# Optimization experiments

Hardware: AMD Instinct MI355X
Metric: run time of the kernel (lower is better)

The kernel has to match this reference:

```python
import jax, jax.numpy as jnp
import numpy as np

N_NODES = 50000
N_EDGES = 600000


def gcn_conv(x, src, dst, W, b, num_nodes):
    # x: [N, Cin] -> [N, Cout]; symmetric-normalized GCN with self-loops
    h = x @ W  # [N, Cout]
    loop = jnp.arange(num_nodes, dtype=src.dtype)
    s = jnp.concatenate([src, loop])
    d = jnp.concatenate([dst, loop])
    ones = jnp.ones(s.shape[0], dtype=h.dtype)
    deg = jax.ops.segment_sum(ones, d, num_segments=num_nodes)  # in-degree incl self-loop
    dinv = jnp.where(deg > 0, jax.lax.rsqrt(deg), 0.0)
    norm = dinv[s] * dinv[d]  # [E+N]
    msg = h[s] * norm[:, None]  # gather + scale
    out = jax.ops.segment_sum(msg, d, num_segments=num_nodes)  # scatter-add
    return out + b


def setup_inputs() -> dict:
    key = jax.random.key(0)
    k1, k2, k3, k4 = jax.random.split(key, 4)
    x = jax.random.normal(k1, (N_NODES, 128), dtype=jnp.float32)
    edge_index = jax.random.randint(k2, (2, N_EDGES), 0, N_NODES, dtype=jnp.int64)
    W1 = jax.random.normal(k3, (128, 128), dtype=jnp.float32) * (1.0 / np.sqrt(128))
    b1 = jnp.zeros((128,), dtype=jnp.float32)
    W2 = jax.random.normal(k4, (128, 64), dtype=jnp.float32) * (1.0 / np.sqrt(128))
    b2 = jnp.zeros((64,), dtype=jnp.float32)
    return {"x": x, "edge_index": edge_index, "W1": W1, "b1": b1, "W2": W2, "b2": b2}


def reference(x, edge_index, W1, b1, W2, b2):
    src, dst = edge_index[0], edge_index[1]
    h = gcn_conv(x, src, dst, W1, b1, N_NODES)
    h = jax.nn.relu(h)
    out = gcn_conv(h, src, dst, W2, b2, N_NODES)
    return out
```

## Files before the change

kernel.cpp:

```cpp
#include <hip/hip_runtime.h>
#include <cstddef>
#include <cstdint>

#define N_NODES 50000
#define N_EDGES 600000
#define M_TILES 3125
#define GEMM_BLKS 782
#define NBUCK 196
#define BUCK_CAP 4096
#define K1_BLKS 147
#define K1_EDGES 4096

typedef short bf16x8 __attribute__((ext_vector_type(8)));
typedef float f32x4 __attribute__((ext_vector_type(4)));


__device__ __forceinline__ unsigned short f32_to_bf16(float x) {
  unsigned u = __float_as_uint(x);
  u += 0x7FFFu + ((u >> 16) & 1u);
  return (unsigned short)(u >> 16);
}
__device__ __forceinline__ float bf16_to_f32(unsigned short h) {
  return __uint_as_float((unsigned)h << 16);
}
__device__ __forceinline__ float bf16_lo(unsigned g) {
  return __uint_as_float(g << 16);
}
__device__ __forceinline__ float bf16_hi(unsigned g) {
  return __uint_as_float(g & 0xFFFF0000u);
}

__device__ __forceinline__ void split8(const float* __restrict__ p, bf16x8& hi,
                                       bf16x8& lo) {
  const float4 v0 = *(const float4*)p;
  const float4 v1 = *(const float4*)(p + 4);
  float v[8] = {v0.x, v0.y, v0.z, v0.w, v1.x, v1.y, v1.z, v1.w};
#pragma unroll
  for (int i = 0; i < 8; i++) {
    const unsigned short h = f32_to_bf16(v[i]);
    hi[i] = (short)h;
    lo[i] = (short)f32_to_bf16(v[i] - bf16_to_f32(h));
  }
}

__global__ __launch_bounds__(256) void k_prep(
    const float* __restrict__ W1, const float* __restrict__ W2,
    unsigned short* __restrict__ w1h, unsigned short* __restrict__ w1l,
    unsigned short* __restrict__ w2h, unsigned short* __restrict__ w2l,
    int* __restrict__ cursor) {
  const int b = blockIdx.x;
  const int tid = threadIdx.x;
  if (b < 96) {
    const int i = b * 256 + tid;
    const float* W;
    unsigned short *wh, *wl;
    int o, cout;
    if (i < 16384) {
      W = W1; wh = w1h; wl = w1l; o = i; cout = 128;
    } else {
      W = W2; wh = w2h; wl = w2l; o = i - 16384; cout = 64;
    }
    const int j = o & 7;
    const int lane = (o >> 3) & 63;
    const int t = o >> 9;
    const int ks = t & 3;
    const int ct = t >> 2;
    const int k = ks * 32 + (lane >> 4) * 8 + j;
    const int n = ct * 16 + (lane & 15);
    const float v = W[k * cout + n];
    const unsigned short h = f32_to_bf16(v);
    wh[o] = h;
    wl[o] = f32_to_bf16(v - bf16_to_f32(h));
  } else {
    if (tid < NBUCK) cursor[tid] = tid * BUCK_CAP;
  }
}

template <int COUT>
__device__ __forceinline__ void gemm_body(const int wtile, const int lane,
                                          const float* __restrict__ X,
                                          const unsigned short* __restrict__ Wph,
                                          const unsigned short* __restrict__ Wpl,
                                          unsigned short* __restrict__ Hs) {
  constexpr int CT = COUT / 16;
  const int m = lane & 15;
  const int q = lane >> 4;

  f32x4 acc[CT];
#pragma unroll
  for (int ct = 0; ct < CT; ct++) acc[ct] = {0.f, 0.f, 0.f, 0.f};

  const float* xp = X + (size_t)(wtile * 16 + m) * 128 + q * 8;

#pragma unroll
  for (int ks = 0; ks < 4; ks++) {
    bf16x8 ah, al;
    split8(xp + ks * 32, ah, al);
#pragma unroll
    for (int ct = 0; ct < CT; ct++) {
      const size_t bo = ((size_t)(ct * 4 + ks) * 64 + lane) * 8;
      const bf16x8 bh = *(const bf16x8*)(Wph + bo);
      const bf16x8 bl = *(const bf16x8*)(Wpl + bo);
      acc[ct] = __builtin_amdgcn_mfma_f32_16x16x32_bf16(ah, bh, acc[ct], 0, 0, 0);
      acc[ct] = __builtin_amdgcn_mfma_f32_16x16x32_bf16(al, bh, acc[ct], 0, 0, 0);
      acc[ct] = __builtin_amdgcn_mfma_f32_16x16x32_bf16(ah, bl, acc[ct], 0, 0, 0);
    }
  }
#pragma unroll
  for (int ct = 0; ct < CT; ct++) {
#pragma unroll
    for (int r = 0; r < 4; r++) {
      const int orow = wtile * 16 + q * 4 + r;
      Hs[(size_t)orow * COUT + ct * 16 + m] = f32_to_bf16(acc[ct][r]);
    }
  }
}

__global__ __launch_bounds__(256) void k_route_gemm128(
    const float* __restrict__ X, const unsigned short* __restrict__ Wph,
    const unsigned short* __restrict__ Wpl, unsigned short* __restrict__ Hs,
    const int* __restrict__ src, const int* __restrict__ dst,
    int* __restrict__ cursor, unsigned* __restrict__ routed) {
  __shared__ int hist[NBUCK];
  __shared__ int lcur[NBUCK];
  const int tid = threadIdx.x;
  if (blockIdx.x < K1_BLKS) {
    for (int t = tid; t < NBUCK; t += 256) hist[t] = 0;
    __syncthreads();
    unsigned packed[16];
    bool cvalid[4];
    const int base = blockIdx.x * K1_EDGES;
#pragma unroll
    for (int c = 0; c < 4; c++) {
      const int i4 = base + c * 1024 + tid * 4;
      cvalid[c] = (i4 < N_EDGES);
      if (cvalid[c]) {
        const int4 d4 = *(const int4*)(dst + i4);
        const int4 s4 = *(const int4*)(src + i4);
        packed[c * 4 + 0] = ((unsigned)d4.x << 16) | (unsigned)s4.x;
        packed[c * 4 + 1] = ((unsigned)d4.y << 16) | (unsigned)s4.y;
        packed[c * 4 + 2] = ((unsigned)d4.z << 16) | (unsigned)s4.z;
        packed[c * 4 + 3] = ((unsigned)d4.w << 16) | (unsigned)s4.w;
#pragma unroll
        for (int j = 0; j < 4; j++)
          atomicAdd(&hist[packed[c * 4 + j] >> 24], 1);
      }
    }
    __syncthreads();
    for (int t = tid; t < NBUCK; t += 256)
      lcur[t] = atomicAdd(&cursor[t], hist[t]);
    __syncthreads();
#pragma unroll
    for (int c = 0; c < 4; c++) {
      if (cvalid[c]) {
#pragma unroll
        for (int j = 0; j < 4; j++) {
          const unsigned pk = packed[c * 4 + j];
          const int slot = atomicAdd(&lcur[pk >> 24], 1);
          routed[slot] = pk;
        }
      }
    }
  } else {
    const int wtile = (blockIdx.x - K1_BLKS) * 4 + (tid >> 6);
    if (wtile < M_TILES) gemm_body<128>(wtile, tid & 63, X, Wph, Wpl, Hs);
  }
}

__global__ __launch_bounds__(1024) void k_bsort(
    const unsigned* __restrict__ routed, const int* __restrict__ cursor,
    int* __restrict__ counts, int* __restrict__ start,
    int* __restrict__ sorted_src) {
  __shared__ unsigned ebuf[BUCK_CAP];
  __shared__ int h2[256];
  __shared__ int c2[256];
  const int b = blockIdx.x;
  const int tid = threadIdx.x;
  const int n = cursor[b] - b * BUCK_CAP;
  for (int i = tid; i < n; i += 1024) ebuf[i] = routed[b * BUCK_CAP + i];
  if (tid < 256) h2[tid] = 0;
  __syncthreads();
  for (int i = tid; i < n; i += 1024)
    atomicAdd(&h2[(ebuf[i] >> 16) & 255], 1);
  __syncthreads();
  int own = 0;
  if (tid < 256) own = h2[tid];
  for (int s = 1; s < 256; s <<= 1) {
    int t = 0;
    if (tid < 256 && tid >= s) t = h2[tid - s];
    __syncthreads();
    if (tid < 256) h2[tid] += t;
    __syncthreads();
  }
  if (tid < 256) {
    const int pfx = h2[tid] - own;
    c2[tid] = pfx;
    const int d = b * 256 + tid;
    if (d < N_NODES) {
      counts[d] = own;
      start[d] = b * BUCK_CAP + pfx;
    }
  }
  __syncthreads();
  for (int i = tid; i < n; i += 1024) {
    const unsigned pk = ebuf[i];
    const int r = atomicAdd(&c2[(pk >> 16) & 255], 1);
    sorted_src[b * BUCK_CAP + r] = (int)(pk & 0xFFFFu);
  }
}

__global__ __launch_bounds__(256) void k_agg128_gemm64(
    const unsigned* __restrict__ Hb, const int* __restrict__ counts,
    const int* __restrict__ start, const int* __restrict__ sorted_src,
    const float* __restrict__ bias, const unsigned short* __restrict__ Wph,
    const unsigned short* __restrict__ Wpl, unsigned short* __restrict__ Hs) {
  __shared__ float a1s[16][132];
  const int lane = threadIdx.x & 63;
  const int wave = threadIdx.x >> 6;
  const float2 bb = ((const float2*)bias)[lane];

  int deg[4], e0v[4];
  float dvv[4];
  unsigned gselfv[4];
  int siv[4];
  float wiv[4];
#pragma unroll
  for (int i = 0; i < 4; i++) {
    const int v = blockIdx.x * 16 + wave * 4 + i;
    deg[i] = counts[v];
    e0v[i] = start[v];
  }
#pragma unroll
  for (int i = 0; i < 4; i++) {
    const int v = blockIdx.x * 16 + wave * 4 + i;
    dvv[i] = rsqrtf((float)deg[i] + 1.0f);
    gselfv[i] = Hb[(size_t)v * 64 + lane];
    siv[i] = (lane < deg[i]) ? sorted_src[e0v[i] + lane] : 0;
  }
#pragma unroll
  for (int i = 0; i < 4; i++) {
    wiv[i] = (lane < deg[i]) ? rsqrtf((float)counts[siv[i]] + 1.0f) * dvv[i]
                             : 0.f;
  }

#pragma unroll
  for (int i = 0; i < 4; i++) {
    const int r = wave * 4 + i;
    const float dv = dvv[i];
    float ax = bf16_lo(gselfv[i]) * (dv * dv);
    float ay = bf16_hi(gselfv[i]) * (dv * dv);
    const int dg = min(deg[i], 64);

    int j = 0;
    for (; j + 8 <= dg; j += 8) {
      int s[8];
      float w[8];
      unsigned g[8];
#pragma unroll
      for (int t = 0; t < 8; t++) {
        s[t] = __shfl(siv[i], j + t);
        w[t] = __shfl(wiv[i], j + t);
      }
#pragma unroll
      for (int t = 0; t < 8; t++) g[t] = Hb[(size_t)s[t] * 64 + lane];
#pragma unroll
      for (int t = 0; t < 8; t++) {
        ax += bf16_lo(g[t]) * w[t];
        ay += bf16_hi(g[t]) * w[t];
      }
    }
    for (; j + 4 <= dg; j += 4) {
      int s[4];
      float w[4];
      unsigned g[4];
#pragma unroll
      for (int t = 0; t < 4; t++) {
        s[t] = __shfl(siv[i], j + t);
        w[t] = __shfl(wiv[i], j + t);
      }
#pragma unroll
      for (int t = 0; t < 4; t++) g[t] = Hb[(size_t)s[t] * 64 + lane];
#pragma unroll
      for (int t = 0; t < 4; t++) {
        ax += bf16_lo(g[t]) * w[t];
        ay += bf16_hi(g[t]) * w[t];
      }
    }
    for (; j < dg; j++) {
      const int s = __shfl(siv[i], j);
      const float w = __shfl(wiv[i], j);
      const unsigned g = Hb[(size_t)s * 64 + lane];
      ax += bf16_lo(g) * w;
      ay += bf16_hi(g) * w;
    }
    a1s[r][lane * 2] = fmaxf(ax + bb.x, 0.f);
    a1s[r][lane * 2 + 1] = fmaxf(ay + bb.y, 0.f);
  }
  __syncthreads();

  const int ct = wave;
  const int m = lane & 15;
  const int q = lane >> 4;
  f32x4 acc = {0.f, 0.f, 0.f, 0.f};
#pragma unroll
  for (int ks = 0; ks < 4; ks++) {
    bf16x8 ah, al;
    split8(&a1s[m][ks * 32 + q * 8], ah, al);
    const size_t bo = ((size_t)(ct * 4 + ks) * 64 + lane) * 8;
    const bf16x8 bh = *(const bf16x8*)(Wph + bo);
    const bf16x8 bl = *(const bf16x8*)(Wpl + bo);
    acc = __builtin_amdgcn_mfma_f32_16x16x32_bf16(ah, bh, acc, 0, 0, 0);
    acc = __builtin_amdgcn_mfma_f32_16x16x32_bf16(al, bh, acc, 0, 0, 0);
    acc = __builtin_amdgcn_mfma_f32_16x16x32_bf16(ah, bl, acc, 0, 0, 0);
  }
#pragma unroll
  for (int r = 0; r < 4; r++) {
    const int orow = blockIdx.x * 16 + q * 4 + r;
    Hs[(size_t)orow * 64 + ct * 16 + m] = f32_to_bf16(acc[r]);
  }
}

__global__ __launch_bounds__(256) void k_agg64(
    const unsigned* __restrict__ Hb, const int* __restrict__ counts,
    const int* __restrict__ start, const int* __restrict__ sorted_src,
    const float* __restrict__ bias, float* __restrict__ out) {
  const int hl = threadIdx.x & 31;
  const int hw = threadIdx.x >> 5;
  const int v0 = blockIdx.x * 16 + hw * 2;
  const float2 bb = ((const float2*)bias)[hl];

  int deg[2], e0v[2];
  float dvv[2];
  unsigned gs[2];
  int siv[2];
  float wiv[2];
#pragma unroll
  for (int i = 0; i < 2; i++) {
    const int v = v0 + i;
    deg[i] = counts[v];
    e0v[i] = start[v];
  }
#pragma unroll
  for (int i = 0; i < 2; i++) {
    const int v = v0 + i;
    dvv[i] = rsqrtf((float)deg[i] + 1.0f);
    gs[i] = Hb[(size_t)v * 32 + hl];
    siv[i] = (hl < deg[i]) ? sorted_src[e0v[i] + hl] : 0;
  }
#pragma unroll
  for (int i = 0; i < 2; i++) {
    wiv[i] = (hl < deg[i]) ? rsqrtf((float)counts[siv[i]] + 1.0f) * dvv[i]
                           : 0.f;
  }

#pragma unroll
  for (int i = 0; i < 2; i++) {
    const int v = v0 + i;
    const float dv = dvv[i];
    float ax = bf16_lo(gs[i]) * (dv * dv);
    float ay = bf16_hi(gs[i]) * (dv * dv);
    const int dg0 = min(deg[i], 32);

    int j = 0;
    for (; j + 8 <= dg0; j += 8) {
      int s[8];
      float w[8];
      unsigned g[8];
#pragma unroll
      for (int t = 0; t < 8; t++) {
        s[t] = __shfl(siv[i], j + t, 32);
        w[t] = __shfl(wiv[i], j + t, 32);
      }
#pragma unroll
      for (int t = 0; t < 8; t++) g[t] = Hb[(size_t)s[t] * 32 + hl];
#pragma unroll
      for (int t = 0; t < 8; t++) {
        ax += bf16_lo(g[t]) * w[t];
        ay += bf16_hi(g[t]) * w[t];
      }
    }
    for (; j + 4 <= dg0; j += 4) {
      int s[4];
      float w[4];
      unsigned g[4];
#pragma unroll
      for (int t = 0; t < 4; t++) {
        s[t] = __shfl(siv[i], j + t, 32);
        w[t] = __shfl(wiv[i], j + t, 32);
      }
#pragma unroll
      for (int t = 0; t < 4; t++) g[t] = Hb[(size_t)s[t] * 32 + hl];
#pragma unroll
      for (int t = 0; t < 4; t++) {
        ax += bf16_lo(g[t]) * w[t];
        ay += bf16_hi(g[t]) * w[t];
      }
    }
    for (; j < dg0; j++) {
      const int s = __shfl(siv[i], j, 32);
      const float w = __shfl(wiv[i], j, 32);
      const unsigned g = Hb[(size_t)s * 32 + hl];
      ax += bf16_lo(g) * w;
      ay += bf16_hi(g) * w;
    }
    for (int base = 32; base < deg[i]; base += 32) {
      const int cnt2 = min(32, deg[i] - base);
      int sit = 0;
      float wit = 0.f;
      if (base + hl < deg[i]) {
        sit = sorted_src[e0v[i] + base + hl];
        wit = rsqrtf((float)counts[sit] + 1.0f) * dv;
      }
      for (int k = 0; k < cnt2; k++) {
        const int s = __shfl(sit, k, 32);
        const float w = __shfl(wit, k, 32);
        const unsigned g = Hb[(size_t)s * 32 + hl];
        ax += bf16_lo(g) * w;
        ay += bf16_hi(g) * w;
      }
    }
    float2 r;
    r.x = ax + bb.x;
    r.y = ay + bb.y;
    ((float2*)out)[(size_t)v * 32 + hl] = r;
  }
}


extern "C" void kernel_launch(void* const* d_in, const int* in_sizes, int n_in,
                              void* d_out, int out_size, void* d_ws, size_t ws_size,
                              hipStream_t stream) {
  const float* x = (const float*)d_in[0];
  const int* ei = (const int*)d_in[1];
  const float* W1 = (const float*)d_in[2];
  const float* b1 = (const float*)d_in[3];
  const float* W2 = (const float*)d_in[4];
  const float* b2 = (const float*)d_in[5];
  const int* src = ei;
  const int* dst = ei + N_EDGES;

  char* p = (char*)d_ws;
  auto alloc = [&](size_t bytes) {
    char* q = p;
    p += (bytes + 255) & ~(size_t)255;
    return q;
  };
  int* cursor = (int*)alloc((size_t)NBUCK * 4);
  unsigned* routed = (unsigned*)alloc((size_t)NBUCK * BUCK_CAP * 4);
  int* sorted_src = (int*)alloc((size_t)NBUCK * BUCK_CAP * 4);
  int* counts = (int*)alloc((size_t)N_NODES * 4);
  int* start = (int*)alloc((size_t)N_NODES * 4);
  unsigned short* w1h = (unsigned short*)alloc(16384 * 2);
  unsigned short* w1l = (unsigned short*)alloc(16384 * 2);
  unsigned short* w2h = (unsigned short*)alloc(8192 * 2);
  unsigned short* w2l = (unsigned short*)alloc(8192 * 2);
  unsigned short* h1b = (unsigned short*)alloc((size_t)N_NODES * 128 * 2);
  unsigned short* h2b = (unsigned short*)alloc((size_t)N_NODES * 64 * 2);

  hipLaunchKernelGGL(k_prep, dim3(97), dim3(256), 0, stream, W1, W2, w1h, w1l,
                     w2h, w2l, cursor);
  hipLaunchKernelGGL(k_route_gemm128, dim3(K1_BLKS + GEMM_BLKS), dim3(256), 0,
                     stream, x, w1h, w1l, h1b, src, dst, cursor, routed);
  hipLaunchKernelGGL(k_bsort, dim3(NBUCK), dim3(1024), 0, stream, routed,
                     cursor, counts, start, sorted_src);
  hipLaunchKernelGGL(k_agg128_gemm64, dim3(M_TILES), dim3(256), 0, stream,
                     (const unsigned*)h1b, counts, start, sorted_src, b1, w2h,
                     w2l, h2b);
  hipLaunchKernelGGL(k_agg64, dim3(M_TILES), dim3(256), 0, stream,
                     (const unsigned*)h2b, counts, start, sorted_src, b2,
                     (float*)d_out);
}
```

Baseline: 152.4 us.

## Regroup kernels: route with prep, bucket sort with layer-1 GEMM, widen aggregation lanes

```diff
diff --git a/kernel.cpp b/kernel.cpp
--- a/kernel.cpp
+++ b/kernel.cpp
@@ -8,8 +8,8 @@
 #define GEMM_BLKS 782
 #define NBUCK 196
 #define BUCK_CAP 4096
-#define K1_BLKS 147
-#define K1_EDGES 4096
+#define ROUTE_EDGES 2048
+#define ROUTE_BLKS 293
 
 typedef short bf16x8 __attribute__((ext_vector_type(8)));
 typedef float f32x4 __attribute__((ext_vector_type(4)));
@@ -43,15 +43,57 @@
   }
 }
 
-__global__ __launch_bounds__(256) void k_prep(
+template <int COUT>
+__device__ __forceinline__ void gemm_body(const int wtile, const int lane,
+                                          const float* __restrict__ X,
+                                          const unsigned short* __restrict__ Wph,
+                                          const unsigned short* __restrict__ Wpl,
+                                          unsigned short* __restrict__ Hs) {
+  constexpr int CT = COUT / 16;
+  const int m = lane & 15;
+  const int q = lane >> 4;
+
+  f32x4 acc[CT];
+#pragma unroll
+  for (int ct = 0; ct < CT; ct++) acc[ct] = {0.f, 0.f, 0.f, 0.f};
+
+  const float* xp = X + (size_t)(wtile * 16 + m) * 128 + q * 8;
+
+#pragma unroll
+  for (int ks = 0; ks < 4; ks++) {
+    bf16x8 ah, al;
+    split8(xp + ks * 32, ah, al);
+#pragma unroll
+    for (int ct = 0; ct < CT; ct++) {
+      const size_t bo = ((size_t)(ct * 4 + ks) * 64 + lane) * 8;
+      const bf16x8 bh = *(const bf16x8*)(Wph + bo);
+      const bf16x8 bl = *(const bf16x8*)(Wpl + bo);
+      acc[ct] = __builtin_amdgcn_mfma_f32_16x16x32_bf16(ah, bh, acc[ct], 0, 0, 0);
+      acc[ct] = __builtin_amdgcn_mfma_f32_16x16x32_bf16(al, bh, acc[ct], 0, 0, 0);
+      acc[ct] = __builtin_amdgcn_mfma_f32_16x16x32_bf16(ah, bl, acc[ct], 0, 0, 0);
+    }
+  }
+#pragma unroll
+  for (int ct = 0; ct < CT; ct++) {
+#pragma unroll
+    for (int r = 0; r < 4; r++) {
+      const int orow = wtile * 16 + q * 4 + r;
+      Hs[(size_t)orow * COUT + ct * 16 + m] = f32_to_bf16(acc[ct][r]);
+    }
+  }
+}
+
+__global__ __launch_bounds__(256) void k_prep_route(
     const float* __restrict__ W1, const float* __restrict__ W2,
     unsigned short* __restrict__ w1h, unsigned short* __restrict__ w1l,
     unsigned short* __restrict__ w2h, unsigned short* __restrict__ w2l,
-    int* __restrict__ cursor) {
-  const int b = blockIdx.x;
+    const int* __restrict__ src, const int* __restrict__ dst,
+    int* __restrict__ cursor, unsigned* __restrict__ routed) {
+  __shared__ int hist[NBUCK];
+  __shared__ int lcur[NBUCK];
   const int tid = threadIdx.x;
-  if (b < 96) {
-    const int i = b * 256 + tid;
+  if (blockIdx.x < 96) {
+    const int i = blockIdx.x * 256 + tid;
     const float* W;
     unsigned short *wh, *wl;
     int o, cout;
@@ -72,66 +114,14 @@
     wh[o] = h;
     wl[o] = f32_to_bf16(v - bf16_to_f32(h));
   } else {
-    if (tid < NBUCK) cursor[tid] = tid * BUCK_CAP;
-  }
-}
-
-template <int COUT>
-__device__ __forceinline__ void gemm_body(const int wtile, const int lane,
-                                          const float* __restrict__ X,
-                                          const unsigned short* __restrict__ Wph,
-                                          const unsigned short* __restrict__ Wpl,
-                                          unsigned short* __restrict__ Hs) {
-  constexpr int CT = COUT / 16;
-  const int m = lane & 15;
-  const int q = lane >> 4;
-
-  f32x4 acc[CT];
-#pragma unroll
-  for (int ct = 0; ct < CT; ct++) acc[ct] = {0.f, 0.f, 0.f, 0.f};
-
-  const float* xp = X + (size_t)(wtile * 16 + m) * 128 + q * 8;
-
-#pragma unroll
-  for (int ks = 0; ks < 4; ks++) {
-    bf16x8 ah, al;
-    split8(xp + ks * 32, ah, al);
-#pragma unroll
-    for (int ct = 0; ct < CT; ct++) {
-      const size_t bo = ((size_t)(ct * 4 + ks) * 64 + lane) * 8;
-      const bf16x8 bh = *(const bf16x8*)(Wph + bo);
-      const bf16x8 bl = *(const bf16x8*)(Wpl + bo);
-      acc[ct] = __builtin_amdgcn_mfma_f32_16x16x32_bf16(ah, bh, acc[ct], 0, 0, 0);
-      acc[ct] = __builtin_amdgcn_mfma_f32_16x16x32_bf16(al, bh, acc[ct], 0, 0, 0);
-      acc[ct] = __builtin_amdgcn_mfma_f32_16x16x32_bf16(ah, bl, acc[ct], 0, 0, 0);
-    }
-  }
-#pragma unroll
-  for (int ct = 0; ct < CT; ct++) {
-#pragma unroll
-    for (int r = 0; r < 4; r++) {
-      const int orow = wtile * 16 + q * 4 + r;
-      Hs[(size_t)orow * COUT + ct * 16 + m] = f32_to_bf16(acc[ct][r]);
-    }
-  }
-}
-
-__global__ __launch_bounds__(256) void k_route_gemm128(
-    const float* __restrict__ X, const unsigned short* __restrict__ Wph,
-    const unsigned short* __restrict__ Wpl, unsigned short* __restrict__ Hs,
-    const int* __restrict__ src, const int* __restrict__ dst,
-    int* __restrict__ cursor, unsigned* __restrict__ routed) {
-  __shared__ int hist[NBUCK];
-  __shared__ int lcur[NBUCK];
-  const int tid = threadIdx.x;
-  if (blockIdx.x < K1_BLKS) {
+    const int rb = blockIdx.x - 96;
     for (int t = tid; t < NBUCK; t += 256) hist[t] = 0;
     __syncthreads();
-    unsigned packed[16];
-    bool cvalid[4];
-    const int base = blockIdx.x * K1_EDGES;
-#pragma unroll
-    for (int c = 0; c < 4; c++) {
+    unsigned packed[8];
+    bool cvalid[2];
+    const int base = rb * ROUTE_EDGES;
+#pragma unroll
+    for (int c = 0; c < 2; c++) {
       const int i4 = base + c * 1024 + tid * 4;
       cvalid[c] = (i4 < N_EDGES);
       if (cvalid[c]) {
@@ -148,10 +138,10 @@
     }
     __syncthreads();
     for (int t = tid; t < NBUCK; t += 256)
-      lcur[t] = atomicAdd(&cursor[t], hist[t]);
-    __syncthreads();
-#pragma unroll
-    for (int c = 0; c < 4; c++) {
+      lcur[t] = t * BUCK_CAP + atomicAdd(&cursor[t], hist[t]);
+    __syncthreads();
+#pragma unroll
+    for (int c = 0; c < 2; c++) {
       if (cvalid[c]) {
 #pragma unroll
         for (int j = 0; j < 4; j++) {
@@ -161,38 +151,35 @@
         }
       }
     }
-  } else {
-    const int wtile = (blockIdx.x - K1_BLKS) * 4 + (tid >> 6);
-    if (wtile < M_TILES) gemm_body<128>(wtile, tid & 63, X, Wph, Wpl, Hs);
-  }
-}
-
-__global__ __launch_bounds__(1024) void k_bsort(
+  }
+}
+
+__global__ __launch_bounds__(256) void k_bsort_gemm128(
     const unsigned* __restrict__ routed, const int* __restrict__ cursor,
     int* __restrict__ counts, int* __restrict__ start,
-    int* __restrict__ sorted_src) {
+    int* __restrict__ sorted_src, const float* __restrict__ X,
+    const unsigned short* __restrict__ Wph,
+    const unsigned short* __restrict__ Wpl, unsigned short* __restrict__ Hs) {
   __shared__ unsigned ebuf[BUCK_CAP];
   __shared__ int h2[256];
   __shared__ int c2[256];
-  const int b = blockIdx.x;
   const int tid = threadIdx.x;
-  const int n = cursor[b] - b * BUCK_CAP;
-  for (int i = tid; i < n; i += 1024) ebuf[i] = routed[b * BUCK_CAP + i];
-  if (tid < 256) h2[tid] = 0;
-  __syncthreads();
-  for (int i = tid; i < n; i += 1024)
-    atomicAdd(&h2[(ebuf[i] >> 16) & 255], 1);
-  __syncthreads();
-  int own = 0;
-  if (tid < 256) own = h2[tid];
-  for (int s = 1; s < 256; s <<= 1) {
-    int t = 0;
-    if (tid < 256 && tid >= s) t = h2[tid - s];
-    __syncthreads();
-    if (tid < 256) h2[tid] += t;
-    __syncthreads();
-  }
-  if (tid < 256) {
+  if (blockIdx.x < NBUCK) {
+    const int b = blockIdx.x;
+    const int n = cursor[b];
+    for (int i = tid; i < n; i += 256) ebuf[i] = routed[b * BUCK_CAP + i];
+    h2[tid] = 0;
+    __syncthreads();
+    for (int i = tid; i < n; i += 256)
+      atomicAdd(&h2[(ebuf[i] >> 16) & 255], 1);
+    __syncthreads();
+    const int own = h2[tid];
+    for (int s = 1; s < 256; s <<= 1) {
+      const int t = (tid >= s) ? h2[tid - s] : 0;
+      __syncthreads();
+      h2[tid] += t;
+      __syncthreads();
+    }
     const int pfx = h2[tid] - own;
     c2[tid] = pfx;
     const int d = b * 256 + tid;
@@ -200,12 +187,15 @@
       counts[d] = own;
       start[d] = b * BUCK_CAP + pfx;
     }
-  }
-  __syncthreads();
-  for (int i = tid; i < n; i += 1024) {
-    const unsigned pk = ebuf[i];
-    const int r = atomicAdd(&c2[(pk >> 16) & 255], 1);
-    sorted_src[b * BUCK_CAP + r] = (int)(pk & 0xFFFFu);
+    __syncthreads();
+    for (int i = tid; i < n; i += 256) {
+      const unsigned pk = ebuf[i];
+      const int r = atomicAdd(&c2[(pk >> 16) & 255], 1);
+      sorted_src[b * BUCK_CAP + r] = (int)(pk & 0xFFFFu);
+    }
+  } else {
+    const int wtile = (blockIdx.x - NBUCK) * 4 + (tid >> 6);
+    if (wtile < M_TILES) gemm_body<128>(wtile, tid & 63, X, Wph, Wpl, Hs);
   }
 }
 
@@ -217,84 +207,78 @@
   __shared__ float a1s[16][132];
   const int lane = threadIdx.x & 63;
   const int wave = threadIdx.x >> 6;
-  const float2 bb = ((const float2*)bias)[lane];
-
-  int deg[4], e0v[4];
-  float dvv[4];
-  unsigned gselfv[4];
-  int siv[4];
-  float wiv[4];
-#pragma unroll
-  for (int i = 0; i < 4; i++) {
-    const int v = blockIdx.x * 16 + wave * 4 + i;
-    deg[i] = counts[v];
-    e0v[i] = start[v];
-  }
-#pragma unroll
-  for (int i = 0; i < 4; i++) {
-    const int v = blockIdx.x * 16 + wave * 4 + i;
-    dvv[i] = rsqrtf((float)deg[i] + 1.0f);
-    gselfv[i] = Hb[(size_t)v * 64 + lane];
-    siv[i] = (lane < deg[i]) ? sorted_src[e0v[i] + lane] : 0;
-  }
-#pragma unroll
-  for (int i = 0; i < 4; i++) {
-    wiv[i] = (lane < deg[i]) ? rsqrtf((float)counts[siv[i]] + 1.0f) * dvv[i]
-                             : 0.f;
-  }
-
-#pragma unroll
-  for (int i = 0; i < 4; i++) {
-    const int r = wave * 4 + i;
-    const float dv = dvv[i];
-    float ax = bf16_lo(gselfv[i]) * (dv * dv);
-    float ay = bf16_hi(gselfv[i]) * (dv * dv);
-    const int dg = min(deg[i], 64);
-
-    int j = 0;
-    for (; j + 8 <= dg; j += 8) {
+  const int h = lane >> 5;
+  const int c = lane & 31;
+  const uint2* __restrict__ Hb2 = (const uint2*)Hb;
+  const float4 bb = ((const float4*)bias)[c];
+  const int vbase = blockIdx.x * 16 + wave * 4;
+
+#pragma unroll
+  for (int p = 0; p < 2; p++) {
+    const int v = vbase + 2 * p + h;
+    const int deg = counts[v];
+    const int e0 = start[v];
+    const float dv = rsqrtf((float)deg + 1.0f);
+    const uint2 gs = Hb2[(size_t)v * 32 + c];
+    int si = 0;
+    float wi = 0.f;
+    if (c < deg) {
+      si = sorted_src[e0 + c];
+      wi = rsqrtf((float)counts[si] + 1.0f) * dv;
+    }
+    const int dA = __shfl(deg, 0);
+    const int dB = __shfl(deg, 32);
+    const int mm = max(dA, dB);
+    const int m = min(mm, 32);
+    const float dv2 = dv * dv;
+    float a0 = bf16_lo(gs.x) * dv2;
+    float a1 = bf16_hi(gs.x) * dv2;
+    float a2 = bf16_lo(gs.y) * dv2;
+    float a3 = bf16_hi(gs.y) * dv2;
+
+    for (int j = 0; j < m; j += 8) {
       int s[8];
       float w[8];
-      unsigned g[8];
+      uint2 g[8];
 #pragma unroll
       for (int t = 0; t < 8; t++) {
-        s[t] = __shfl(siv[i], j + t);
-        w[t] = __shfl(wiv[i], j + t);
-      }
-#pragma unroll
-      for (int t = 0; t < 8; t++) g[t] = Hb[(size_t)s[t] * 64 + lane];
+        s[t] = __shfl(si, (lane & 32) | (j + t));
+        w[t] = __shfl(wi, (lane & 32) | (j + t));
+      }
+#pragma unroll
+      for (int t = 0; t < 8; t++) g[t] = Hb2[(size_t)s[t] * 32 + c];
 #pragma unroll
       for (int t = 0; t < 8; t++) {
-        ax += bf16_lo(g[t]) * w[t];
-        ay += bf16_hi(g[t]) * w[t];
-      }
-    }
-    for (; j + 4 <= dg; j += 4) {
-      int s[4];
-      float w[4];
-      unsigned g[4];
-#pragma unroll
-      for (int t = 0; t < 4; t++) {
-        s[t] = __shfl(siv[i], j + t);
-        w[t] = __shfl(wiv[i], j + t);
-      }
-#pragma unroll
-      for (int t = 0; t < 4; t++) g[t] = Hb[(size_t)s[t] * 64 + lane];
-#pragma unroll
-      for (int t = 0; t < 4; t++) {
-        ax += bf16_lo(g[t]) * w[t];
-        ay += bf16_hi(g[t]) * w[t];
-      }
-    }
-    for (; j < dg; j++) {
-      const int s = __shfl(siv[i], j);
-      const float w = __shfl(wiv[i], j);
-      const unsigned g = Hb[(size_t)s * 64 + lane];
-      ax += bf16_lo(g) * w;
-      ay += bf16_hi(g) * w;
-    }
-    a1s[r][lane * 2] = fmaxf(ax + bb.x, 0.f);
-    a1s[r][lane * 2 + 1] = fmaxf(ay + bb.y, 0.f);
+        a0 += bf16_lo(g[t].x) * w[t];
+        a1 += bf16_hi(g[t].x) * w[t];
+        a2 += bf16_lo(g[t].y) * w[t];
+        a3 += bf16_hi(g[t].y) * w[t];
+      }
+    }
+    for (int base = 32; base < mm; base += 32) {
+      int sit = 0;
+      float wit = 0.f;
+      if (base + c < deg) {
+        sit = sorted_src[e0 + base + c];
+        wit = rsqrtf((float)counts[sit] + 1.0f) * dv;
+      }
+      const int lim = min(32, mm - base);
+      for (int k = 0; k < lim; k++) {
+        const int s = __shfl(sit, (lane & 32) | k);
+        const float w = __shfl(wit, (lane & 32) | k);
+        const uint2 g = Hb2[(size_t)s * 32 + c];
+        a0 += bf16_lo(g.x) * w;
+        a1 += bf16_hi(g.x) * w;
+        a2 += bf16_lo(g.y) * w;
+        a3 += bf16_hi(g.y) * w;
+      }
+    }
+    float4 r;
+    r.x = fmaxf(a0 + bb.x, 0.f);
+    r.y = fmaxf(a1 + bb.y, 0.f);
+    r.z = fmaxf(a2 + bb.z, 0.f);
+    r.w = fmaxf(a3 + bb.w, 0.f);
+    *(float4*)&a1s[wave * 4 + 2 * p + h][c * 4] = r;
   }
   __syncthreads();
 
@@ -324,106 +308,88 @@
     const unsigned* __restrict__ Hb, const int* __restrict__ counts,
     const int* __restrict__ start, const int* __restrict__ sorted_src,
     const float* __restrict__ bias, float* __restrict__ out) {
-  const int hl = threadIdx.x & 31;
-  const int hw = threadIdx.x >> 5;
-  const int v0 = blockIdx.x * 16 + hw * 2;
-  const float2 bb = ((const float2*)bias)[hl];
-
-  int deg[2], e0v[2];
-  float dvv[2];
-  unsigned gs[2];
-  int siv[2];
-  float wiv[2];
-#pragma unroll
-  for (int i = 0; i < 2; i++) {
-    const int v = v0 + i;
-    deg[i] = counts[v];
-    e0v[i] = start[v];
-  }
-#pragma unroll
-  for (int i = 0; i < 2; i++) {
-    const int v = v0 + i;
-    dvv[i] = rsqrtf((float)deg[i] + 1.0f);
-    gs[i] = Hb[(size_t)v * 32 + hl];
-    siv[i] = (hl < deg[i]) ? sorted_src[e0v[i] + hl] : 0;
-  }
-#pragma unroll
-  for (int i = 0; i < 2; i++) {
-    wiv[i] = (hl < deg[i]) ? rsqrtf((float)counts[siv[i]] + 1.0f) * dvv[i]
-                           : 0.f;
-  }
-
-#pragma unroll
-  for (int i = 0; i < 2; i++) {
-    const int v = v0 + i;
-    const float dv = dvv[i];
-    float ax = bf16_lo(gs[i]) * (dv * dv);
-    float ay = bf16_hi(gs[i]) * (dv * dv);
-    const int dg0 = min(deg[i], 32);
-
-    int j = 0;
-    for (; j + 8 <= dg0; j += 8) {
+  const int lane = threadIdx.x & 63;
+  const int wave = threadIdx.x >> 6;
+  const int qq = lane >> 4;
+  const int c = lane & 15;
+  const uint2* __restrict__ Hb2 = (const uint2*)Hb;
+  const float4 bb = ((const float4*)bias)[c];
+
+  const int v = blockIdx.x * 16 + wave * 4 + qq;
+  const int deg = counts[v];
+  const int e0 = start[v];
+  const float dv = rsqrtf((float)deg + 1.0f);
+  const uint2 gs = Hb2[(size_t)v * 16 + c];
+  int si0 = 0, si1 = 0;
+  float wi0 = 0.f, wi1 = 0.f;
+  if (c < deg) {
+    si0 = sorted_src[e0 + c];
+    wi0 = rsqrtf((float)counts[si0] + 1.0f) * dv;
+  }
+  if (c + 16 < deg) {
+    si1 = sorted_src[e0 + c + 16];
+    wi1 = rsqrtf((float)counts[si1] + 1.0f) * dv;
+  }
+  const int d0 = __shfl(deg, 0);
+  const int d1 = __shfl(deg, 16);
+  const int d2 = __shfl(deg, 32);
+  const int d3 = __shfl(deg, 48);
+  const int mm = max(max(d0, d1), max(d2, d3));
+  const int m = min(mm, 32);
+  const float dv2 = dv * dv;
+  float a0 = bf16_lo(gs.x) * dv2;
+  float a1 = bf16_hi(gs.x) * dv2;
+  float a2 = bf16_lo(gs.y) * dv2;
+  float a3 = bf16_hi(gs.y) * dv2;
+
+#pragma unroll
+  for (int jb = 0; jb < 4; jb++) {
+    if (jb * 8 < m) {
       int s[8];
       float w[8];
-      unsigned g[8];
+      uint2 g[8];
 #pragma unroll
       for (int t = 0; t < 8; t++) {
-        s[t] = __shfl(siv[i], j + t, 32);
-        w[t] = __shfl(wiv[i], j + t, 32);
-      }
-#pragma unroll
-      for (int t = 0; t < 8; t++) g[t] = Hb[(size_t)s[t] * 32 + hl];
+        const int e = jb * 8 + t;
+        const int srcl = (lane & 48) | (e & 15);
+        s[t] = __shfl((jb < 2) ? si0 : si1, srcl);
+        w[t] = __shfl((jb < 2) ? wi0 : wi1, srcl);
+      }
+#pragma unroll
+      for (int t = 0; t < 8; t++) g[t] = Hb2[(size_t)s[t] * 16 + c];
 #pragma unroll
       for (int t = 0; t < 8; t++) {
-        ax += bf16_lo(g[t]) * w[t];
-        ay += bf16_hi(g[t]) * w[t];
-      }
-    }
-    for (; j + 4 <= dg0; j += 4) {
-      int s[4];
-      float w[4];
-      unsigned g[4];
-#pragma unroll
-      for (int t = 0; t < 4; t++) {
-        s[t] = __shfl(siv[i], j + t, 32);
-        w[t] = __shfl(wiv[i], j + t, 32);
-      }
-#pragma unroll
-      for (int t = 0; t < 4; t++) g[t] = Hb[(size_t)s[t] * 32 + hl];
-#pragma unroll
-      for (int t = 0; t < 4; t++) {
-        ax += bf16_lo(g[t]) * w[t];
-        ay += bf16_hi(g[t]) * w[t];
-      }
-    }
-    for (; j < dg0; j++) {
-      const int s = __shfl(siv[i], j, 32);
-      const float w = __shfl(wiv[i], j, 32);
-      const unsigned g = Hb[(size_t)s * 32 + hl];
-      ax += bf16_lo(g) * w;
-      ay += bf16_hi(g) * w;
-    }
-    for (int base = 32; base < deg[i]; base += 32) {
-      const int cnt2 = min(32, deg[i] - base);
-      int sit = 0;
-      float wit = 0.f;
-      if (base + hl < deg[i]) {
-        sit = sorted_src[e0v[i] + base + hl];
-        wit = rsqrtf((float)counts[sit] + 1.0f) * dv;
-      }
-      for (int k = 0; k < cnt2; k++) {
-        const int s = __shfl(sit, k, 32);
-        const float w = __shfl(wit, k, 32);
-        const unsigned g = Hb[(size_t)s * 32 + hl];
-        ax += bf16_lo(g) * w;
-        ay += bf16_hi(g) * w;
-      }
-    }
-    float2 r;
-    r.x = ax + bb.x;
-    r.y = ay + bb.y;
-    ((float2*)out)[(size_t)v * 32 + hl] = r;
-  }
+        a0 += bf16_lo(g[t].x) * w[t];
+        a1 += bf16_hi(g[t].x) * w[t];
+        a2 += bf16_lo(g[t].y) * w[t];
+        a3 += bf16_hi(g[t].y) * w[t];
+      }
+    }
+  }
+  for (int base = 32; base < mm; base += 16) {
+    int sit = 0;
+    float wit = 0.f;
+    if (base + c < deg) {
+      sit = sorted_src[e0 + base + c];
+      wit = rsqrtf((float)counts[sit] + 1.0f) * dv;
+    }
+    const int lim = min(16, mm - base);
+    for (int k = 0; k < lim; k++) {
+      const int s = __shfl(sit, (lane & 48) | k);
+      const float w = __shfl(wit, (lane & 48) | k);
+      const uint2 g = Hb2[(size_t)s * 16 + c];
+      a0 += bf16_lo(g.x) * w;
+      a1 += bf16_hi(g.x) * w;
+      a2 += bf16_lo(g.y) * w;
+      a3 += bf16_hi(g.y) * w;
+    }
+  }
+  float4 r;
+  r.x = a0 + bb.x;
+  r.y = a1 + bb.y;
+  r.z = a2 + bb.z;
+  r.w = a3 + bb.w;
+  ((float4*)out)[(size_t)v * 16 + c] = r;
 }
 
 
@@ -457,12 +423,12 @@
   unsigned short* h1b = (unsigned short*)alloc((size_t)N_NODES * 128 * 2);
   unsigned short* h2b = (unsigned short*)alloc((size_t)N_NODES * 64 * 2);
 
-  hipLaunchKernelGGL(k_prep, dim3(97), dim3(256), 0, stream, W1, W2, w1h, w1l,
-                     w2h, w2l, cursor);
-  hipLaunchKernelGGL(k_route_gemm128, dim3(K1_BLKS + GEMM_BLKS), dim3(256), 0,
-                     stream, x, w1h, w1l, h1b, src, dst, cursor, routed);
-  hipLaunchKernelGGL(k_bsort, dim3(NBUCK), dim3(1024), 0, stream, routed,
-                     cursor, counts, start, sorted_src);
+  hipMemsetAsync(cursor, 0, (size_t)NBUCK * 4, stream);
+  hipLaunchKernelGGL(k_prep_route, dim3(96 + ROUTE_BLKS), dim3(256), 0, stream,
+                     W1, W2, w1h, w1l, w2h, w2l, src, dst, cursor, routed);
+  hipLaunchKernelGGL(k_bsort_gemm128, dim3(NBUCK + GEMM_BLKS), dim3(256), 0,
+                     stream, routed, cursor, counts, start, sorted_src, x, w1h,
+                     w1l, h1b);
   hipLaunchKernelGGL(k_agg128_gemm64, dim3(M_TILES), dim3(256), 0, stream,
                      (const unsigned*)h1b, counts, start, sorted_src, b1, w2h,
                      w2l, h2b);
```

Measured after the change: 152.9 us. Within noise of the previous version (+0.3%).
